# Kernel optimization log

Measured on AMD Instinct MI355X. Metric: run time of the kernel, lower is better.

## Reference

```python
import jax, jax.numpy as jnp
import numpy as np

RTOL, ATOL = 1e-3, 1e-6
MAX_STEPS = 20          # fixed upper bound on adaptive steps (masked scan)
TA, TB, TC = 1.0, 1.0, 0.0  # trig basis params a, b, c from basis_str
B, DIN, DT, DOUT = 512, 512, 512, 512


def _rms(x):
    return jnp.sqrt(jnp.mean(x * x))


def _ode_f(t, A, C):
    # Basis.trig: stack([sin(a*A + b*t + c), cos(a*A + b*t + c)], -1) -> [B, DT, 2]
    phase = TA * A + TB * t + TC
    basis = jnp.stack([jnp.sin(phase), jnp.cos(phase)], axis=-1)
    # tensordot(A_basis, C, dims=([1,2], [1,2])): contract tensor dims + basis dim
    return jnp.einsum('bjk,ijk->bi', basis, C)


def _rk45(C, y0, t0, t1):
    """scipy-style adaptive RK45 (Dormand-Prince) from t0 to t1, fixed-length masked scan."""
    f = lambda t, y: _ode_f(t, y, C)
    f0 = f(t0, y0)
    # --- scipy _select_initial_step ---
    scale0 = ATOL + RTOL * jnp.abs(y0)
    d0 = _rms(y0 / scale0)
    d1 = _rms(f0 / scale0)
    h0 = jnp.where((d0 < 1e-5) | (d1 < 1e-5), jnp.float32(1e-6), 0.01 * d0 / d1)
    f1 = f(t0 + h0, y0 + h0 * f0)
    d2 = _rms((f1 - f0) / scale0) / h0
    dmax = jnp.maximum(d1, d2)
    h1 = jnp.where(dmax <= 1e-15, jnp.maximum(jnp.float32(1e-6), h0 * 1e-3), (0.01 / dmax) ** 0.2)
    h_init = jnp.minimum(jnp.minimum(100.0 * h0, h1), t1 - t0)

    def step(carry, _):
        t, y, fy, h, done = carry
        hs = jnp.minimum(h, t1 - t)
        k1 = fy
        k2 = f(t + hs * (1.0 / 5.0), y + hs * (k1 * (1.0 / 5.0)))
        k3 = f(t + hs * (3.0 / 10.0), y + hs * (3.0 / 40.0 * k1 + 9.0 / 40.0 * k2))
        k4 = f(t + hs * (4.0 / 5.0), y + hs * (44.0 / 45.0 * k1 - 56.0 / 15.0 * k2 + 32.0 / 9.0 * k3))
        k5 = f(t + hs * (8.0 / 9.0), y + hs * (19372.0 / 6561.0 * k1 - 25360.0 / 2187.0 * k2
                                               + 64448.0 / 6561.0 * k3 - 212.0 / 729.0 * k4))
        k6 = f(t + hs, y + hs * (9017.0 / 3168.0 * k1 - 355.0 / 33.0 * k2 + 46732.0 / 5247.0 * k3
                                 + 49.0 / 176.0 * k4 - 5103.0 / 18656.0 * k5))
        y_new = y + hs * (35.0 / 384.0 * k1 + 500.0 / 1113.0 * k3 + 125.0 / 192.0 * k4
                          - 2187.0 / 6784.0 * k5 + 11.0 / 84.0 * k6)
        k7 = f(t + hs, y_new)  # FSAL stage
        err = hs * (71.0 / 57600.0 * k1 - 71.0 / 16695.0 * k3 + 71.0 / 1920.0 * k4
                    - 17253.0 / 339200.0 * k5 + 22.0 / 525.0 * k6 - 1.0 / 40.0 * k7)
        sc = ATOL + RTOL * jnp.maximum(jnp.abs(y), jnp.abs(y_new))
        en = _rms(err / sc)
        accept = en < 1.0
        safe = jnp.maximum(en, 1e-10)
        fac = jnp.where(accept,
                        jnp.minimum(10.0, 0.9 * safe ** -0.2),
                        jnp.maximum(0.2, 0.9 * safe ** -0.2))
        t_n = jnp.where(accept, t + hs, t)
        y_n = jnp.where(accept, y_new, y)
        f_n = jnp.where(accept, k7, fy)
        h_n = hs * fac
        reached = t_n >= t1 - 1e-7
        # freeze state once integration is finished
        t_o = jnp.where(done, t, t_n)
        y_o = jnp.where(done, y, y_n)
        f_o = jnp.where(done, fy, f_n)
        h_o = jnp.where(done, h, h_n)
        return (t_o, y_o, f_o, h_o, done | reached), None

    init = (jnp.float32(t0), y0, f0, h_init.astype(jnp.float32), jnp.array(False))
    (tf, yf, _, _, _), _ = jax.lax.scan(step, init, None, length=MAX_STEPS)
    return yf


def setup_inputs() -> dict:
    key = jax.random.key(0)
    kx, kp, kc, kf = jax.random.split(key, 4)
    x = jax.random.normal(kx, (B, DIN), dtype=jnp.float32)
    P = jax.random.uniform(kp, (DIN, DT), dtype=jnp.float32, minval=0.01, maxval=1.0)
    # scale C so dA/dt stays O(1) at DT=512 (pure rescaling of the Uniform init)
    C = jax.random.uniform(kc, (DT, DT, 2), dtype=jnp.float32, minval=0.01, maxval=1.0) / (DT * 2)
    F = jax.random.uniform(kf, (DT, DOUT), dtype=jnp.float32, minval=0.01, maxval=1.0)
    return {"x": x, "P": P, "C": C, "F": F}


def reference(x, P, C, F):
    # A0 = tensordot(x, P) over input dims
    A0 = jnp.einsum('bi,ij->bj', x, P)
    Af = _rk45(C, A0, jnp.float32(0.0), jnp.float32(1.0))
    # y_hat = tensordot(A_f, F) over tensor dims
    return jnp.einsum('bj,jo->bo', Af, F)
```

## Files before the change

### kernel.cpp

```cpp
#include <hip/hip_runtime.h>
#include <cmath>

typedef float floatx4 __attribute__((ext_vector_type(4)));
typedef __bf16 bf16x8 __attribute__((ext_vector_type(8)));

#define NDT 512
#define NEL (512 * 512)
#define NELF 262144.0f

#define AF0_OFF 65536
#define AF1_OFF (65536 + 262144)
#define YF_OFF (65536 + 2 * 262144)
#define BFC_OFF (YF_OFF + 131072)
#define BFP_OFF (BFC_OFF + 262144)
#define BFF_OFF (BFP_OFF + 131072)

#define RTOLc 1e-3f
#define ATOLc 1e-6f
#define TAc 1.0f
#define TBc 1.0f
#define TCc 0.0f

union UB { uint4 u; bf16x8 v; };
union UB2 { unsigned long long q[2]; uint4 u; bf16x8 v; };

__device__ __forceinline__ uint32_t f2bf(float f) {
  uint32_t u = __float_as_uint(f);
  return (u + 0x7fffu + ((u >> 16) & 1u)) >> 16;
}

#define AST(p, v) __hip_atomic_store((p), (v), __ATOMIC_RELAXED, __HIP_MEMORY_SCOPE_AGENT)
#define ALD(p) __hip_atomic_load((p), __ATOMIC_RELAXED, __HIP_MEMORY_SCOPE_AGENT)

__global__ __launch_bounds__(256) void pack_all(const float* __restrict__ C,
                                                const float* __restrict__ P,
                                                const float* __restrict__ F,
                                                __bf16* __restrict__ BfC,
                                                unsigned short* __restrict__ BfP,
                                                unsigned short* __restrict__ BfF,
                                                unsigned* __restrict__ ctl) {
  const int bid = blockIdx.x, tid = threadIdx.x;
  if (bid == 0) {
    for (int i = tid; i < 4096; i += 256) ctl[i] = 0u;
  }
  if (bid < 512) {
    int t = bid * 256 + tid;
    int i = t >> 8;
    int pr = t & 255;
    floatx4 v = *(const floatx4*)(C + (size_t)i * 1024 + pr * 4);
    uint32_t w0 = f2bf(v[0]) | (f2bf(v[1]) << 16);
    uint32_t w1 = f2bf(v[2]) | (f2bf(v[3]) << 16);
    int c0 = i >> 4;
    int kc = pr >> 3;
    int lq = (pr >> 1) & 3;
    int ln = (i & 15) | (lq << 4);
    int jp = (pr & 1) * 4;
    uint2 val; val.x = w0; val.y = w1;
    *(uint2*)(BfC + ((size_t)(c0 * 32 + kc) * 64 + ln) * 8 + jp) = val;
  } else {
    const float* M = (bid < 768) ? P : F;
    unsigned short* Bf = (bid < 768) ? BfP : BfF;
    int t = ((bid < 768) ? (bid - 512) : (bid - 768)) * 256 + tid;
    int idx = t * 4;
    int k = idx >> 9;
    int n0 = idx & 511;
    floatx4 v = *(const floatx4*)(M + (size_t)k * NDT + n0);
    int kc = k >> 5;
    int lq = (k >> 3) & 3;
    int j = k & 7;
#pragma unroll
    for (int i = 0; i < 4; ++i) {
      int n = n0 + i;
      int nf = n >> 4;
      int lane = (n & 15) | (lq << 4);
      Bf[((size_t)(nf * 16 + kc) * 64 + lane) * 8 + j] = (unsigned short)f2bf(v[i]);
    }
  }
}

__global__ __launch_bounds__(256, 1) void ode_mfma(const float* __restrict__ x,
                                                   float* __restrict__ out,
                                                   float* __restrict__ ws) {
  __shared__ __align__(16) float red[4][16][68];
  __shared__ __align__(16) unsigned short ldsX[16 * 64 * 8];
  __shared__ float bred[4];
  __shared__ float shb0s, shb1s;

  unsigned* CNT = (unsigned*)ws;
  unsigned* RCNT = ((unsigned*)ws) + 1024;
  float* PART1 = ws + 4096;
  float* PART2 = ws + 16384;
  unsigned long long* AfA = (unsigned long long*)(ws + AF0_OFF);
  unsigned long long* AfB = (unsigned long long*)(ws + AF1_OFF);
  unsigned long long* YF = (unsigned long long*)(ws + YF_OFF);
  const __bf16* Bf = (const __bf16*)(ws + BFC_OFF);
  const __bf16* BfP = (const __bf16*)(ws + BFP_OFF);
  const __bf16* BfF = (const __bf16*)(ws + BFF_OFF);

  const int tid = threadIdx.x;
  const int lane = tid & 63;
  const int w = tid >> 6;
  const int cb = blockIdx.x >> 5;
  const int rg = blockIdx.x & 31;
  const int rl = tid & 15;
  const int gcq = cb * 16 + (tid >> 4);

  UB Breg[4][8];
#pragma unroll
  for (int cf = 0; cf < 4; ++cf)
#pragma unroll
    for (int i = 0; i < 8; ++i)
      Breg[cf][i].u =
          *(const uint4*)(Bf + (((size_t)(cb * 4 + cf) * 32 + 8 * w + i) * 64 + lane) * 8);

  int rg_phase = 0, par = 0;

  auto rg_barrier = [&]() {
    __syncthreads();
    ++rg_phase;
    if (tid == 0) {
      __hip_atomic_fetch_add(&CNT[rg * 32], 1u, __ATOMIC_RELAXED, __HIP_MEMORY_SCOPE_AGENT);
      while (ALD(&CNT[rg * 32]) < 8u * (unsigned)rg_phase) __builtin_amdgcn_s_sleep(1);
    }
    __syncthreads();
  };

  auto reduce4 = [&](floatx4 a0, floatx4 a1, floatx4 a2, floatx4 a3) -> floatx4 {
    __syncthreads();
    const int q = lane >> 4, l4 = lane & 15;
#pragma unroll
    for (int ri = 0; ri < 4; ++ri) {
      red[w][4 * q + ri][l4] = a0[ri];
      red[w][4 * q + ri][16 + l4] = a1[ri];
      red[w][4 * q + ri][32 + l4] = a2[ri];
      red[w][4 * q + ri][48 + l4] = a3[ri];
    }
    __syncthreads();
    const int c0 = (tid >> 4) * 4;
    floatx4 o = *(const floatx4*)&red[0][rl][c0];
    o += *(const floatx4*)&red[1][rl][c0];
    o += *(const floatx4*)&red[2][rl][c0];
    o += *(const floatx4*)&red[3][rl][c0];
    return o;
  };

  const int kcw = gcq >> 2;
  const int alw = rl | ((gcq & 3) << 4);
  const size_t wslot = ((size_t)(rg * 32 + kcw) * 64 + alw) * 2;

  auto write_basis = [&](floatx4 av, float targ) {
    uint32_t d[4];
#pragma unroll
    for (int e = 0; e < 4; ++e) {
      float s, c;
      __sincosf(TAc * av[e] + targ, &s, &c);
      d[e] = f2bf(s) | (f2bf(c) << 16);
    }
    unsigned long long* Ap = (par ? AfB : AfA) + wslot;
    AST(Ap, (unsigned long long)d[0] | ((unsigned long long)d[1] << 32));
    AST(Ap + 1, (unsigned long long)d[2] | ((unsigned long long)d[3] << 32));
  };

  auto gemm = [&]() -> floatx4 {
    const unsigned long long* Ap =
        (par ? AfB : AfA) + ((size_t)(rg * 32 + 8 * w) * 64 + lane) * 2;
    UB2 a[8];
#pragma unroll
    for (int i = 0; i < 8; ++i) {
      a[i].q[0] = ALD(Ap + (size_t)i * 128);
      a[i].q[1] = ALD(Ap + (size_t)i * 128 + 1);
    }
    floatx4 acc0 = {0.f, 0.f, 0.f, 0.f}, acc1 = acc0, acc2 = acc0, acc3 = acc0;
#pragma unroll
    for (int i = 0; i < 8; ++i) {
      acc0 = __builtin_amdgcn_mfma_f32_16x16x32_bf16(a[i].v, Breg[0][i].v, acc0, 0, 0, 0);
      acc1 = __builtin_amdgcn_mfma_f32_16x16x32_bf16(a[i].v, Breg[1][i].v, acc1, 0, 0, 0);
      acc2 = __builtin_amdgcn_mfma_f32_16x16x32_bf16(a[i].v, Breg[2][i].v, acc2, 0, 0, 0);
      acc3 = __builtin_amdgcn_mfma_f32_16x16x32_bf16(a[i].v, Breg[3][i].v, acc3, 0, 0, 0);
    }
    par ^= 1;
    return reduce4(acc0, acc1, acc2, acc3);
  };

  auto block_sum = [&](float v) -> float {
#pragma unroll
    for (int o = 32; o; o >>= 1) v += __shfl_down(v, o, 64);
    __syncthreads();
    if (lane == 0) bred[w] = v;
    __syncthreads();
    return (tid == 0) ? (bred[0] + bred[1] + bred[2] + bred[3]) : 0.0f;
  };

  auto grid_reduce = [&](float va, float vb, int sa, int sb, bool two) -> float2 {
    float ba = block_sum(va);
    float bb = two ? block_sum(vb) : 0.0f;
    ++rg_phase;
    if (tid == 0) {
      AST(&PART1[sa * 256 + rg * 8 + cb], ba);
      if (two) AST(&PART1[sb * 256 + rg * 8 + cb], bb);
      asm volatile("s_waitcnt vmcnt(0)" ::: "memory");
      __hip_atomic_fetch_add(&CNT[rg * 32], 1u, __ATOMIC_RELAXED, __HIP_MEMORY_SCOPE_AGENT);
    }
    if (cb == 0 && tid == 0) {
      while (ALD(&CNT[rg * 32]) < 8u * (unsigned)rg_phase) __builtin_amdgcn_s_sleep(1);
      float ra = 0.f, rb = 0.f;
#pragma unroll
      for (int i = 0; i < 8; ++i) ra += ALD(&PART1[sa * 256 + rg * 8 + i]);
      AST(&PART2[(size_t)(sa * 32 + rg) * 32], ra);
      if (two) {
#pragma unroll
        for (int i = 0; i < 8; ++i) rb += ALD(&PART1[sb * 256 + rg * 8 + i]);
        AST(&PART2[(size_t)(sb * 32 + rg) * 32], rb);
      }
      asm volatile("s_waitcnt vmcnt(0)" ::: "memory");
      __hip_atomic_fetch_add(&RCNT[sa * 32], 1u, __ATOMIC_RELAXED, __HIP_MEMORY_SCOPE_AGENT);
    }
    if (tid == 0) {
      while (ALD(&RCNT[sa * 32]) < 32u) __builtin_amdgcn_s_sleep(1);
    }
    __syncthreads();
    if (w == 0) {
      float x0 = (lane < 32) ? ALD(&PART2[(size_t)(sa * 32 + lane) * 32]) : 0.0f;
      float x1 = (two && lane < 32) ? ALD(&PART2[(size_t)(sb * 32 + lane) * 32]) : 0.0f;
#pragma unroll
      for (int o = 16; o; o >>= 1) {
        x0 += __shfl_down(x0, o, 32);
        x1 += __shfl_down(x1, o, 32);
      }
      if (lane == 0) { shb0s = x0; shb1s = x1; }
    }
    __syncthreads();
    return make_float2(shb0s, shb1s);
  };

  floatx4 y, fy, k2, k3, k4, k5, k6, k7, yn, av;
  {
    for (int idx = tid; idx < 8192; idx += 256) {
      int r = idx >> 9, k = idx & 511;
      float v = x[(size_t)(rg * 16 + r) * NDT + k];
      int al = r | (((k >> 3) & 3) << 4);
      ldsX[((size_t)(k >> 5) * 64 + al) * 8 + (k & 7)] = (unsigned short)f2bf(v);
    }
    __syncthreads();
    floatx4 a0 = {0.f, 0.f, 0.f, 0.f}, a1 = a0, a2 = a0, a3 = a0;
#pragma unroll
    for (int i = 0; i < 4; ++i) {
      UB a, b;
      a.u = *(const uint4*)(ldsX + ((size_t)(4 * w + i) * 64 + lane) * 8);
      b.u = *(const uint4*)(BfP + (((size_t)(cb * 4 + 0) * 16 + 4 * w + i) * 64 + lane) * 8);
      a0 = __builtin_amdgcn_mfma_f32_16x16x32_bf16(a.v, b.v, a0, 0, 0, 0);
      b.u = *(const uint4*)(BfP + (((size_t)(cb * 4 + 1) * 16 + 4 * w + i) * 64 + lane) * 8);
      a1 = __builtin_amdgcn_mfma_f32_16x16x32_bf16(a.v, b.v, a1, 0, 0, 0);
      b.u = *(const uint4*)(BfP + (((size_t)(cb * 4 + 2) * 16 + 4 * w + i) * 64 + lane) * 8);
      a2 = __builtin_amdgcn_mfma_f32_16x16x32_bf16(a.v, b.v, a2, 0, 0, 0);
      b.u = *(const uint4*)(BfP + (((size_t)(cb * 4 + 3) * 16 + 4 * w + i) * 64 + lane) * 8);
      a3 = __builtin_amdgcn_mfma_f32_16x16x32_bf16(a.v, b.v, a3, 0, 0, 0);
    }
    y = reduce4(a0, a1, a2, a3);
  }

  write_basis(y, TCc + TBc * 0.0f);
  rg_barrier();
  fy = gemm();
  {
    float s0 = 0.f, s1 = 0.f;
#pragma unroll
    for (int r = 0; r < 4; ++r) {
      float sv = ATOLc + RTOLc * fabsf(y[r]);
      float a = y[r] / sv, b = fy[r] / sv;
      s0 += a * a;
      s1 += b * b;
    }
    float2 d01 = grid_reduce(s0, s1, 0, 1, true);
    const float d0 = sqrtf(d01.x / NELF);
    const float d1 = sqrtf(d01.y / NELF);
    const float h0 = (d0 < 1e-5f || d1 < 1e-5f) ? 1e-6f : 0.01f * d0 / d1;
    av = y + h0 * fy;
    write_basis(av, TCc + TBc * h0);
    rg_barrier();
    k2 = gemm();
    float s2 = 0.f;
#pragma unroll
    for (int r = 0; r < 4; ++r) {
      float sv = ATOLc + RTOLc * fabsf(y[r]);
      float dd = (k2[r] - fy[r]) / sv;
      s2 += dd * dd;
    }
    const float d2 = sqrtf(grid_reduce(s2, 0.f, 2, 0, false).x / NELF) / h0;
    const float dmax = fmaxf(d1, d2);
    const float h1i = (dmax <= 1e-15f) ? fmaxf(1e-6f, h0 * 1e-3f) : powf(0.01f / dmax, 0.2f);
    float h = fminf(fminf(100.0f * h0, h1i), 1.0f);
    float t = 0.0f;
    bool done = false;
    int it = 0;

    const float a21 = (float)(1.0 / 5.0);
    const float a31 = (float)(3.0 / 40.0), a32 = (float)(9.0 / 40.0);
    const float a41 = (float)(44.0 / 45.0), a42 = (float)(-56.0 / 15.0), a43 = (float)(32.0 / 9.0);
    const float a51 = (float)(19372.0 / 6561.0), a52 = (float)(-25360.0 / 2187.0),
                a53 = (float)(64448.0 / 6561.0), a54 = (float)(-212.0 / 729.0);
    const float a61 = (float)(9017.0 / 3168.0), a62 = (float)(-355.0 / 33.0),
                a63 = (float)(46732.0 / 5247.0), a64 = (float)(49.0 / 176.0),
                a65 = (float)(-5103.0 / 18656.0);
    const float b1 = (float)(35.0 / 384.0), b3 = (float)(500.0 / 1113.0),
                b4 = (float)(125.0 / 192.0), b5 = (float)(-2187.0 / 6784.0),
                b6 = (float)(11.0 / 84.0);
    const float e1c = (float)(71.0 / 57600.0), e3c = (float)(-71.0 / 16695.0),
                e4c = (float)(71.0 / 1920.0), e5c = (float)(-17253.0 / 339200.0),
                e6c = (float)(22.0 / 525.0), e7c = (float)(-1.0 / 40.0);
    const float c89 = (float)(8.0 / 9.0);

    while (true) {
      const float hs = fminf(h, 1.0f - t);

      av = y + (hs * a21) * fy;
      write_basis(av, TCc + TBc * (t + 0.2f * hs));
      rg_barrier();
      k2 = gemm();

      av = y + hs * (a31 * fy + a32 * k2);
      write_basis(av, TCc + TBc * (t + 0.3f * hs));
      rg_barrier();
      k3 = gemm();

      av = y + hs * (a41 * fy + a42 * k2 + a43 * k3);
      write_basis(av, TCc + TBc * (t + 0.8f * hs));
      rg_barrier();
      k4 = gemm();

      av = y + hs * (a51 * fy + a52 * k2 + a53 * k3 + a54 * k4);
      write_basis(av, TCc + TBc * (t + c89 * hs));
      rg_barrier();
      k5 = gemm();

      av = y + hs * (a61 * fy + a62 * k2 + a63 * k3 + a64 * k4 + a65 * k5);
      write_basis(av, TCc + TBc * (t + hs));
      rg_barrier();
      k6 = gemm();

      yn = y + hs * (b1 * fy + b3 * k3 + b4 * k4 + b5 * k5 + b6 * k6);
      write_basis(yn, TCc + TBc * (t + hs));
      rg_barrier();
      k7 = gemm();

      float es = 0.f;
#pragma unroll
      for (int r = 0; r < 4; ++r) {
        float errc = hs * (e1c * fy[r] + e3c * k3[r] + e4c * k4[r] + e5c * k5[r] + e6c * k6[r] +
                           e7c * k7[r]);
        float sv = ATOLc + RTOLc * fmaxf(fabsf(y[r]), fabsf(yn[r]));
        float dd = errc / sv;
        es += dd * dd;
      }
      const float en = sqrtf(grid_reduce(es, 0.f, 3 + it, 0, false).x / NELF);
      const bool accept = en < 1.0f;
      const float safe = fmaxf(en, 1e-10f);
      float fac = 0.9f * powf(safe, -0.2f);
      fac = accept ? fminf(10.0f, fac) : fmaxf(0.2f, fac);
      if (accept) {
        t = t + hs;
        y = yn;
        fy = k7;
      }
      h = hs * fac;
      done = done || (t >= 1.0f - 1e-7f);
      ++it;
      if (done || it >= 20) break;
    }
  }

  {
    uint32_t d0 = f2bf(y[0]) | (f2bf(y[1]) << 16);
    uint32_t d1 = f2bf(y[2]) | (f2bf(y[3]) << 16);
    const int kcF = gcq >> 3;
    const int alF = rl | (((gcq >> 1) & 3) << 4);
    AST(YF + ((size_t)(rg * 16 + kcF) * 64 + alF) * 2 + (gcq & 1),
        (unsigned long long)d0 | ((unsigned long long)d1 << 32));
  }
  rg_barrier();
  {
    floatx4 a0 = {0.f, 0.f, 0.f, 0.f}, a1 = a0, a2 = a0, a3 = a0;
#pragma unroll
    for (int i = 0; i < 4; ++i) {
      UB2 a;
      const size_t base = ((size_t)(rg * 16 + 4 * w + i) * 64 + lane) * 2;
      a.q[0] = ALD(YF + base);
      a.q[1] = ALD(YF + base + 1);
      UB b;
      b.u = *(const uint4*)(BfF + (((size_t)(cb * 4 + 0) * 16 + 4 * w + i) * 64 + lane) * 8);
      a0 = __builtin_amdgcn_mfma_f32_16x16x32_bf16(a.v, b.v, a0, 0, 0, 0);
      b.u = *(const uint4*)(BfF + (((size_t)(cb * 4 + 1) * 16 + 4 * w + i) * 64 + lane) * 8);
      a1 = __builtin_amdgcn_mfma_f32_16x16x32_bf16(a.v, b.v, a1, 0, 0, 0);
      b.u = *(const uint4*)(BfF + (((size_t)(cb * 4 + 2) * 16 + 4 * w + i) * 64 + lane) * 8);
      a2 = __builtin_amdgcn_mfma_f32_16x16x32_bf16(a.v, b.v, a2, 0, 0, 0);
      b.u = *(const uint4*)(BfF + (((size_t)(cb * 4 + 3) * 16 + 4 * w + i) * 64 + lane) * 8);
      a3 = __builtin_amdgcn_mfma_f32_16x16x32_bf16(a.v, b.v, a3, 0, 0, 0);
    }
    floatx4 o = reduce4(a0, a1, a2, a3);
    *(floatx4*)(out + (size_t)(rg * 16 + rl) * NDT + cb * 64 + (tid >> 4) * 4) = o;
  }
}

extern "C" void kernel_launch(void* const* d_in, const int* in_sizes, int n_in,
                              void* d_out, int out_size, void* d_ws, size_t ws_size,
                              hipStream_t stream) {
  (void)in_sizes; (void)n_in; (void)out_size; (void)ws_size;
  const float* x = (const float*)d_in[0];
  const float* P = (const float*)d_in[1];
  const float* C = (const float*)d_in[2];
  const float* F = (const float*)d_in[3];
  float* out = (float*)d_out;
  float* ws = (float*)d_ws;

  hipLaunchKernelGGL(pack_all, dim3(1024), dim3(256), 0, stream, C, P, F,
                     (__bf16*)(ws + BFC_OFF), (unsigned short*)(ws + BFP_OFF),
                     (unsigned short*)(ws + BFF_OFF), (unsigned*)ws);
  hipLaunchKernelGGL(ode_mfma, dim3(256), dim3(256), 0, stream, x, out, ws);
}
```

Measured before the change: 149.6 us.

## Fuse bf16 packing into ODE kernel and replace atomic counters with per-block flags

Removes the separate packing kernel. Each block now converts its slice of C into bf16 MFMA register fragments on the fly, and P and F are gathered and converted inside the GEMM loops. The row-group barrier changes from atomic-add counters to per-block phase flags that are written with plain stores and polled by 8 threads, which avoids atomic contention. The costs are strided scalar loads of P and F, read straight from fp32 global memory, and a small control-zeroing kernel launch.

```diff
diff --git a/kernel.cpp b/kernel.cpp
--- a/kernel.cpp
+++ b/kernel.cpp
@@ -5,15 +5,11 @@
 typedef __bf16 bf16x8 __attribute__((ext_vector_type(8)));
 
 #define NDT 512
-#define NEL (512 * 512)
 #define NELF 262144.0f
 
 #define AF0_OFF 65536
 #define AF1_OFF (65536 + 262144)
 #define YF_OFF (65536 + 2 * 262144)
-#define BFC_OFF (YF_OFF + 131072)
-#define BFP_OFF (BFC_OFF + 262144)
-#define BFF_OFF (BFP_OFF + 131072)
 
 #define RTOLc 1e-3f
 #define ATOLc 1e-6f
@@ -32,53 +28,14 @@
 #define AST(p, v) __hip_atomic_store((p), (v), __ATOMIC_RELAXED, __HIP_MEMORY_SCOPE_AGENT)
 #define ALD(p) __hip_atomic_load((p), __ATOMIC_RELAXED, __HIP_MEMORY_SCOPE_AGENT)
 
-__global__ __launch_bounds__(256) void pack_all(const float* __restrict__ C,
-                                                const float* __restrict__ P,
-                                                const float* __restrict__ F,
-                                                __bf16* __restrict__ BfC,
-                                                unsigned short* __restrict__ BfP,
-                                                unsigned short* __restrict__ BfF,
-                                                unsigned* __restrict__ ctl) {
-  const int bid = blockIdx.x, tid = threadIdx.x;
-  if (bid == 0) {
-    for (int i = tid; i < 4096; i += 256) ctl[i] = 0u;
-  }
-  if (bid < 512) {
-    int t = bid * 256 + tid;
-    int i = t >> 8;
-    int pr = t & 255;
-    floatx4 v = *(const floatx4*)(C + (size_t)i * 1024 + pr * 4);
-    uint32_t w0 = f2bf(v[0]) | (f2bf(v[1]) << 16);
-    uint32_t w1 = f2bf(v[2]) | (f2bf(v[3]) << 16);
-    int c0 = i >> 4;
-    int kc = pr >> 3;
-    int lq = (pr >> 1) & 3;
-    int ln = (i & 15) | (lq << 4);
-    int jp = (pr & 1) * 4;
-    uint2 val; val.x = w0; val.y = w1;
-    *(uint2*)(BfC + ((size_t)(c0 * 32 + kc) * 64 + ln) * 8 + jp) = val;
-  } else {
-    const float* M = (bid < 768) ? P : F;
-    unsigned short* Bf = (bid < 768) ? BfP : BfF;
-    int t = ((bid < 768) ? (bid - 512) : (bid - 768)) * 256 + tid;
-    int idx = t * 4;
-    int k = idx >> 9;
-    int n0 = idx & 511;
-    floatx4 v = *(const floatx4*)(M + (size_t)k * NDT + n0);
-    int kc = k >> 5;
-    int lq = (k >> 3) & 3;
-    int j = k & 7;
-#pragma unroll
-    for (int i = 0; i < 4; ++i) {
-      int n = n0 + i;
-      int nf = n >> 4;
-      int lane = (n & 15) | (lq << 4);
-      Bf[((size_t)(nf * 16 + kc) * 64 + lane) * 8 + j] = (unsigned short)f2bf(v[i]);
-    }
-  }
+__global__ __launch_bounds__(256) void ctl_zero(unsigned* __restrict__ ctl) {
+  for (int i = threadIdx.x; i < 8192; i += 256) ctl[i] = 0u;
 }
 
 __global__ __launch_bounds__(256, 1) void ode_mfma(const float* __restrict__ x,
+                                                   const float* __restrict__ C,
+                                                   const float* __restrict__ P,
+                                                   const float* __restrict__ F,
                                                    float* __restrict__ out,
                                                    float* __restrict__ ws) {
   __shared__ __align__(16) float red[4][16][68];
@@ -86,16 +43,13 @@
   __shared__ float bred[4];
   __shared__ float shb0s, shb1s;
 
-  unsigned* CNT = (unsigned*)ws;
-  unsigned* RCNT = ((unsigned*)ws) + 1024;
-  float* PART1 = ws + 4096;
+  unsigned* FLAG = (unsigned*)ws;
+  unsigned* RCNT = ((unsigned*)ws) + 4096;
+  float* PART1 = ws + 8192;
   float* PART2 = ws + 16384;
   unsigned long long* AfA = (unsigned long long*)(ws + AF0_OFF);
   unsigned long long* AfB = (unsigned long long*)(ws + AF1_OFF);
   unsigned long long* YF = (unsigned long long*)(ws + YF_OFF);
-  const __bf16* Bf = (const __bf16*)(ws + BFC_OFF);
-  const __bf16* BfP = (const __bf16*)(ws + BFP_OFF);
-  const __bf16* BfF = (const __bf16*)(ws + BFF_OFF);
 
   const int tid = threadIdx.x;
   const int lane = tid & 63;
@@ -105,22 +59,30 @@
   const int rl = tid & 15;
   const int gcq = cb * 16 + (tid >> 4);
 
+  const int nbase = cb * 64 + (lane & 15);
+  const int kq8 = ((lane >> 4) & 3) * 8;
+
   UB Breg[4][8];
 #pragma unroll
   for (int cf = 0; cf < 4; ++cf)
 #pragma unroll
-    for (int i = 0; i < 8; ++i)
+    for (int i = 0; i < 8; ++i) {
+      const float* cp = C + (size_t)(nbase + cf * 16) * 1024 + (8 * w + i) * 32 + kq8;
+      floatx4 v0 = *(const floatx4*)cp;
+      floatx4 v1 = *(const floatx4*)(cp + 4);
       Breg[cf][i].u =
-          *(const uint4*)(Bf + (((size_t)(cb * 4 + cf) * 32 + 8 * w + i) * 64 + lane) * 8);
+          make_uint4(f2bf(v0[0]) | (f2bf(v0[1]) << 16), f2bf(v0[2]) | (f2bf(v0[3]) << 16),
+                     f2bf(v1[0]) | (f2bf(v1[1]) << 16), f2bf(v1[2]) | (f2bf(v1[3]) << 16));
+    }
 
   int rg_phase = 0, par = 0;
 
   auto rg_barrier = [&]() {
     __syncthreads();
     ++rg_phase;
-    if (tid == 0) {
-      __hip_atomic_fetch_add(&CNT[rg * 32], 1u, __ATOMIC_RELAXED, __HIP_MEMORY_SCOPE_AGENT);
-      while (ALD(&CNT[rg * 32]) < 8u * (unsigned)rg_phase) __builtin_amdgcn_s_sleep(1);
+    if (tid == 0) AST(&FLAG[(rg * 8 + cb) * 8], (unsigned)rg_phase);
+    if (tid < 8) {
+      while (ALD(&FLAG[(rg * 8 + tid) * 8]) < (unsigned)rg_phase) __builtin_amdgcn_s_sleep(1);
     }
     __syncthreads();
   };
@@ -199,10 +161,13 @@
       AST(&PART1[sa * 256 + rg * 8 + cb], ba);
       if (two) AST(&PART1[sb * 256 + rg * 8 + cb], bb);
       asm volatile("s_waitcnt vmcnt(0)" ::: "memory");
-      __hip_atomic_fetch_add(&CNT[rg * 32], 1u, __ATOMIC_RELAXED, __HIP_MEMORY_SCOPE_AGENT);
-    }
+      AST(&FLAG[(rg * 8 + cb) * 8], (unsigned)rg_phase);
+    }
+    if (cb == 0 && tid < 8) {
+      while (ALD(&FLAG[(rg * 8 + tid) * 8]) < (unsigned)rg_phase) __builtin_amdgcn_s_sleep(1);
+    }
+    __syncthreads();
     if (cb == 0 && tid == 0) {
-      while (ALD(&CNT[rg * 32]) < 8u * (unsigned)rg_phase) __builtin_amdgcn_s_sleep(1);
       float ra = 0.f, rb = 0.f;
 #pragma unroll
       for (int i = 0; i < 8; ++i) ra += ALD(&PART1[sa * 256 + rg * 8 + i]);
@@ -231,6 +196,21 @@
     }
     __syncthreads();
     return make_float2(shb0s, shb1s);
+  };
+
+  auto load_b512 = [&](const float* M, int Kb, int cf) -> UB {
+    const float* pp = M + (size_t)Kb * NDT + nbase + cf * 16;
+    uint32_t e0 = f2bf(pp[0]);
+    uint32_t e1 = f2bf(pp[512]);
+    uint32_t e2 = f2bf(pp[1024]);
+    uint32_t e3 = f2bf(pp[1536]);
+    uint32_t e4 = f2bf(pp[2048]);
+    uint32_t e5 = f2bf(pp[2560]);
+    uint32_t e6 = f2bf(pp[3072]);
+    uint32_t e7 = f2bf(pp[3584]);
+    UB b;
+    b.u = make_uint4(e0 | (e1 << 16), e2 | (e3 << 16), e4 | (e5 << 16), e6 | (e7 << 16));
+    return b;
   };
 
   floatx4 y, fy, k2, k3, k4, k5, k6, k7, yn, av;
@@ -245,16 +225,13 @@
     floatx4 a0 = {0.f, 0.f, 0.f, 0.f}, a1 = a0, a2 = a0, a3 = a0;
 #pragma unroll
     for (int i = 0; i < 4; ++i) {
-      UB a, b;
+      UB a;
       a.u = *(const uint4*)(ldsX + ((size_t)(4 * w + i) * 64 + lane) * 8);
-      b.u = *(const uint4*)(BfP + (((size_t)(cb * 4 + 0) * 16 + 4 * w + i) * 64 + lane) * 8);
-      a0 = __builtin_amdgcn_mfma_f32_16x16x32_bf16(a.v, b.v, a0, 0, 0, 0);
-      b.u = *(const uint4*)(BfP + (((size_t)(cb * 4 + 1) * 16 + 4 * w + i) * 64 + lane) * 8);
-      a1 = __builtin_amdgcn_mfma_f32_16x16x32_bf16(a.v, b.v, a1, 0, 0, 0);
-      b.u = *(const uint4*)(BfP + (((size_t)(cb * 4 + 2) * 16 + 4 * w + i) * 64 + lane) * 8);
-      a2 = __builtin_amdgcn_mfma_f32_16x16x32_bf16(a.v, b.v, a2, 0, 0, 0);
-      b.u = *(const uint4*)(BfP + (((size_t)(cb * 4 + 3) * 16 + 4 * w + i) * 64 + lane) * 8);
-      a3 = __builtin_amdgcn_mfma_f32_16x16x32_bf16(a.v, b.v, a3, 0, 0, 0);
+      const int Kb = (4 * w + i) * 32 + kq8;
+      a0 = __builtin_amdgcn_mfma_f32_16x16x32_bf16(a.v, load_b512(P, Kb, 0).v, a0, 0, 0, 0);
+      a1 = __builtin_amdgcn_mfma_f32_16x16x32_bf16(a.v, load_b512(P, Kb, 1).v, a1, 0, 0, 0);
+      a2 = __builtin_amdgcn_mfma_f32_16x16x32_bf16(a.v, load_b512(P, Kb, 2).v, a2, 0, 0, 0);
+      a3 = __builtin_amdgcn_mfma_f32_16x16x32_bf16(a.v, load_b512(P, Kb, 3).v, a3, 0, 0, 0);
     }
     y = reduce4(a0, a1, a2, a3);
   }
@@ -386,15 +363,11 @@
       const size_t base = ((size_t)(rg * 16 + 4 * w + i) * 64 + lane) * 2;
       a.q[0] = ALD(YF + base);
       a.q[1] = ALD(YF + base + 1);
-      UB b;
-      b.u = *(const uint4*)(BfF + (((size_t)(cb * 4 + 0) * 16 + 4 * w + i) * 64 + lane) * 8);
-      a0 = __builtin_amdgcn_mfma_f32_16x16x32_bf16(a.v, b.v, a0, 0, 0, 0);
-      b.u = *(const uint4*)(BfF + (((size_t)(cb * 4 + 1) * 16 + 4 * w + i) * 64 + lane) * 8);
-      a1 = __builtin_amdgcn_mfma_f32_16x16x32_bf16(a.v, b.v, a1, 0, 0, 0);
-      b.u = *(const uint4*)(BfF + (((size_t)(cb * 4 + 2) * 16 + 4 * w + i) * 64 + lane) * 8);
-      a2 = __builtin_amdgcn_mfma_f32_16x16x32_bf16(a.v, b.v, a2, 0, 0, 0);
-      b.u = *(const uint4*)(BfF + (((size_t)(cb * 4 + 3) * 16 + 4 * w + i) * 64 + lane) * 8);
-      a3 = __builtin_amdgcn_mfma_f32_16x16x32_bf16(a.v, b.v, a3, 0, 0, 0);
+      const int Kb = (4 * w + i) * 32 + kq8;
+      a0 = __builtin_amdgcn_mfma_f32_16x16x32_bf16(a.v, load_b512(F, Kb, 0).v, a0, 0, 0, 0);
+      a1 = __builtin_amdgcn_mfma_f32_16x16x32_bf16(a.v, load_b512(F, Kb, 1).v, a1, 0, 0, 0);
+      a2 = __builtin_amdgcn_mfma_f32_16x16x32_bf16(a.v, load_b512(F, Kb, 2).v, a2, 0, 0, 0);
+      a3 = __builtin_amdgcn_mfma_f32_16x16x32_bf16(a.v, load_b512(F, Kb, 3).v, a3, 0, 0, 0);
     }
     floatx4 o = reduce4(a0, a1, a2, a3);
     *(floatx4*)(out + (size_t)(rg * 16 + rl) * NDT + cb * 64 + (tid >> 4) * 4) = o;
@@ -412,8 +385,6 @@
   float* out = (float*)d_out;
   float* ws = (float*)d_ws;
 
-  hipLaunchKernelGGL(pack_all, dim3(1024), dim3(256), 0, stream, C, P, F,
-                     (__bf16*)(ws + BFC_OFF), (unsigned short*)(ws + BFP_OFF),
-                     (unsigned short*)(ws + BFF_OFF), (unsigned*)ws);
-  hipLaunchKernelGGL(ode_mfma, dim3(256), dim3(256), 0, stream, x, out, ws);
+  hipLaunchKernelGGL(ctl_zero, dim3(1), dim3(256), 0, stream, (unsigned*)ws);
+  hipLaunchKernelGGL(ode_mfma, dim3(256), dim3(256), 0, stream, x, C, P, F, out, ws);
 }
```

Measured after the change: 173.5 us. 1.16x slower.

## Replace atomic-counter barriers with per-block flags and single-level grid reduction

Applied to the files above, without the earlier changes.

Row-group barriers and grid reductions now use per-block monotonic flags that each block stores, instead of atomic fetch-add counters. The two-level reduction, where a leader block gathers partials and publishes them, becomes a direct read of all 256 partials by wave 0 of every block. The P/F pack kernel is rewritten so each thread gathers 8 K-values and does one 16-byte store instead of scattered 2-byte stores, cutting its grid from 1024 to 768 blocks. YF now aliases the AfA buffer, which shrinks the workspace but relies on that buffer being dead by the time YF is written.

```diff
diff --git a/kernel.cpp b/kernel.cpp
--- a/kernel.cpp
+++ b/kernel.cpp
@@ -5,13 +5,11 @@
 typedef __bf16 bf16x8 __attribute__((ext_vector_type(8)));
 
 #define NDT 512
-#define NEL (512 * 512)
 #define NELF 262144.0f
 
-#define AF0_OFF 65536
-#define AF1_OFF (65536 + 262144)
-#define YF_OFF (65536 + 2 * 262144)
-#define BFC_OFF (YF_OFF + 131072)
+#define AF0_OFF 16384
+#define AF1_OFF (16384 + 262144)
+#define BFC_OFF (16384 + 2 * 262144)
 #define BFP_OFF (BFC_OFF + 262144)
 #define BFF_OFF (BFP_OFF + 131072)
 
@@ -36,8 +34,8 @@
                                                 const float* __restrict__ P,
                                                 const float* __restrict__ F,
                                                 __bf16* __restrict__ BfC,
-                                                unsigned short* __restrict__ BfP,
-                                                unsigned short* __restrict__ BfF,
+                                                unsigned* __restrict__ BfP,
+                                                unsigned* __restrict__ BfF,
                                                 unsigned* __restrict__ ctl) {
   const int bid = blockIdx.x, tid = threadIdx.x;
   if (bid == 0) {
@@ -58,23 +56,25 @@
     uint2 val; val.x = w0; val.y = w1;
     *(uint2*)(BfC + ((size_t)(c0 * 32 + kc) * 64 + ln) * 8 + jp) = val;
   } else {
-    const float* M = (bid < 768) ? P : F;
-    unsigned short* Bf = (bid < 768) ? BfP : BfF;
-    int t = ((bid < 768) ? (bid - 512) : (bid - 768)) * 256 + tid;
-    int idx = t * 4;
-    int k = idx >> 9;
-    int n0 = idx & 511;
-    floatx4 v = *(const floatx4*)(M + (size_t)k * NDT + n0);
-    int kc = k >> 5;
-    int lq = (k >> 3) & 3;
-    int j = k & 7;
-#pragma unroll
-    for (int i = 0; i < 4; ++i) {
-      int n = n0 + i;
-      int nf = n >> 4;
-      int lane = (n & 15) | (lq << 4);
-      Bf[((size_t)(nf * 16 + kc) * 64 + lane) * 8 + j] = (unsigned short)f2bf(v[i]);
-    }
+    const float* M = (bid < 640) ? P : F;
+    unsigned* Bf = (bid < 640) ? BfP : BfF;
+    int t = ((bid < 640) ? (bid - 512) : (bid - 640)) * 256 + tid;
+    int lane = t & 63;
+    int kc = (t >> 6) & 15;
+    int nf = t >> 10;
+    int n = nf * 16 + (lane & 15);
+    int K0 = kc * 32 + ((lane >> 4) & 3) * 8;
+    const float* mp = M + (size_t)K0 * NDT + n;
+    uint32_t e0 = f2bf(mp[0]);
+    uint32_t e1 = f2bf(mp[512]);
+    uint32_t e2 = f2bf(mp[1024]);
+    uint32_t e3 = f2bf(mp[1536]);
+    uint32_t e4 = f2bf(mp[2048]);
+    uint32_t e5 = f2bf(mp[2560]);
+    uint32_t e6 = f2bf(mp[3072]);
+    uint32_t e7 = f2bf(mp[3584]);
+    *(uint4*)(Bf + ((size_t)(nf * 16 + kc) * 64 + lane) * 4) =
+        make_uint4(e0 | (e1 << 16), e2 | (e3 << 16), e4 | (e5 << 16), e6 | (e7 << 16));
   }
 }
 
@@ -86,13 +86,11 @@
   __shared__ float bred[4];
   __shared__ float shb0s, shb1s;
 
-  unsigned* CNT = (unsigned*)ws;
-  unsigned* RCNT = ((unsigned*)ws) + 1024;
+  unsigned* FLAG = (unsigned*)ws;
   float* PART1 = ws + 4096;
-  float* PART2 = ws + 16384;
   unsigned long long* AfA = (unsigned long long*)(ws + AF0_OFF);
   unsigned long long* AfB = (unsigned long long*)(ws + AF1_OFF);
-  unsigned long long* YF = (unsigned long long*)(ws + YF_OFF);
+  unsigned long long* YF = (unsigned long long*)(ws + AF0_OFF);
   const __bf16* Bf = (const __bf16*)(ws + BFC_OFF);
   const __bf16* BfP = (const __bf16*)(ws + BFP_OFF);
   const __bf16* BfF = (const __bf16*)(ws + BFF_OFF);
@@ -104,6 +102,7 @@
   const int rg = blockIdx.x & 31;
   const int rl = tid & 15;
   const int gcq = cb * 16 + (tid >> 4);
+  const int blk = rg * 8 + cb;
 
   UB Breg[4][8];
 #pragma unroll
@@ -118,9 +117,9 @@
   auto rg_barrier = [&]() {
     __syncthreads();
     ++rg_phase;
-    if (tid == 0) {
-      __hip_atomic_fetch_add(&CNT[rg * 32], 1u, __ATOMIC_RELAXED, __HIP_MEMORY_SCOPE_AGENT);
-      while (ALD(&CNT[rg * 32]) < 8u * (unsigned)rg_phase) __builtin_amdgcn_s_sleep(1);
+    if (tid == 0) AST(&FLAG[blk * 8], (unsigned)rg_phase);
+    if (tid < 8) {
+      while (ALD(&FLAG[(rg * 8 + tid) * 8]) < (unsigned)rg_phase) __builtin_amdgcn_s_sleep(1);
     }
     __syncthreads();
   };
@@ -196,36 +195,27 @@
     float bb = two ? block_sum(vb) : 0.0f;
     ++rg_phase;
     if (tid == 0) {
-      AST(&PART1[sa * 256 + rg * 8 + cb], ba);
-      if (two) AST(&PART1[sb * 256 + rg * 8 + cb], bb);
+      AST(&PART1[sa * 256 + blk], ba);
+      if (two) AST(&PART1[sb * 256 + blk], bb);
       asm volatile("s_waitcnt vmcnt(0)" ::: "memory");
-      __hip_atomic_fetch_add(&CNT[rg * 32], 1u, __ATOMIC_RELAXED, __HIP_MEMORY_SCOPE_AGENT);
-    }
-    if (cb == 0 && tid == 0) {
-      while (ALD(&CNT[rg * 32]) < 8u * (unsigned)rg_phase) __builtin_amdgcn_s_sleep(1);
-      float ra = 0.f, rb = 0.f;
-#pragma unroll
-      for (int i = 0; i < 8; ++i) ra += ALD(&PART1[sa * 256 + rg * 8 + i]);
-      AST(&PART2[(size_t)(sa * 32 + rg) * 32], ra);
-      if (two) {
-#pragma unroll
-        for (int i = 0; i < 8; ++i) rb += ALD(&PART1[sb * 256 + rg * 8 + i]);
-        AST(&PART2[(size_t)(sb * 32 + rg) * 32], rb);
+      AST(&FLAG[blk * 8], (unsigned)rg_phase);
+    }
+    if (w == 0) {
+#pragma unroll
+      for (int k = 0; k < 4; ++k) {
+        while (ALD(&FLAG[(lane + 64 * k) * 8]) < (unsigned)rg_phase)
+          __builtin_amdgcn_s_sleep(1);
       }
-      asm volatile("s_waitcnt vmcnt(0)" ::: "memory");
-      __hip_atomic_fetch_add(&RCNT[sa * 32], 1u, __ATOMIC_RELAXED, __HIP_MEMORY_SCOPE_AGENT);
-    }
-    if (tid == 0) {
-      while (ALD(&RCNT[sa * 32]) < 32u) __builtin_amdgcn_s_sleep(1);
-    }
-    __syncthreads();
-    if (w == 0) {
-      float x0 = (lane < 32) ? ALD(&PART2[(size_t)(sa * 32 + lane) * 32]) : 0.0f;
-      float x1 = (two && lane < 32) ? ALD(&PART2[(size_t)(sb * 32 + lane) * 32]) : 0.0f;
-#pragma unroll
-      for (int o = 16; o; o >>= 1) {
-        x0 += __shfl_down(x0, o, 32);
-        x1 += __shfl_down(x1, o, 32);
+      float x0 = ALD(&PART1[sa * 256 + lane]) + ALD(&PART1[sa * 256 + lane + 64]) +
+                 ALD(&PART1[sa * 256 + lane + 128]) + ALD(&PART1[sa * 256 + lane + 192]);
+      float x1 = 0.0f;
+      if (two)
+        x1 = ALD(&PART1[sb * 256 + lane]) + ALD(&PART1[sb * 256 + lane + 64]) +
+             ALD(&PART1[sb * 256 + lane + 128]) + ALD(&PART1[sb * 256 + lane + 192]);
+#pragma unroll
+      for (int o = 32; o; o >>= 1) {
+        x0 += __shfl_down(x0, o, 64);
+        x1 += __shfl_down(x1, o, 64);
       }
       if (lane == 0) { shb0s = x0; shb1s = x1; }
     }
@@ -412,8 +402,8 @@
   float* out = (float*)d_out;
   float* ws = (float*)d_ws;
 
-  hipLaunchKernelGGL(pack_all, dim3(1024), dim3(256), 0, stream, C, P, F,
-                     (__bf16*)(ws + BFC_OFF), (unsigned short*)(ws + BFP_OFF),
-                     (unsigned short*)(ws + BFF_OFF), (unsigned*)ws);
+  hipLaunchKernelGGL(pack_all, dim3(768), dim3(256), 0, stream, C, P, F,
+                     (__bf16*)(ws + BFC_OFF), (unsigned*)(ws + BFP_OFF),
+                     (unsigned*)(ws + BFF_OFF), (unsigned*)ws);
   hipLaunchKernelGGL(ode_mfma, dim3(256), dim3(256), 0, stream, x, out, ws);
 }
```

After: 142.6 us. 4.7% less time.
